# Optimization experiments

Measured on AMD Instinct MI355X. Metric: run time of the kernel, lower is better.

Reference implementation:

```python
import jax, jax.numpy as jnp
import numpy as np

SEQ_LEN = 8192
SIGMA = 2.0
COUNT_WEIGHT = 0.1
PEAK_PROB = 0.002  # ~16 peaks per sequence
LOG_CLAMP = -100.0  # torch F.binary_cross_entropy clamps log to -100


def setup_inputs() -> dict:
    key = jax.random.key(0)
    k1, k2 = jax.random.split(key)
    B = 32
    pred = jax.random.uniform(k1, (B, SEQ_LEN, 1), dtype=jnp.float32,
                              minval=1e-6, maxval=1.0 - 1e-6)
    # sparse binary peak indicator, as in radar pulse labels
    target = (jax.random.uniform(k2, (B, SEQ_LEN, 1)) < PEAK_PROB).astype(jnp.float32)
    return {"pred": pred, "target": target}


def _gaussian_target(target):
    # target: [B, T, 1]; original loops over every (b, t) peak and adds a
    # full-length gaussian centered at t. Vectorized: mask[B,T] @ K[T,T].
    T = target.shape[1]
    t_idx = jnp.arange(T, dtype=jnp.float32)
    K = jnp.exp(-0.5 * ((t_idx[None, :] - t_idx[:, None]) / SIGMA) ** 2)  # [T, T]
    mask = (target[:, :, 0] > 0).astype(jnp.float32)                      # [B, T]
    g = jnp.einsum("bt,ts->bs", mask, K)                                  # [B, T]
    return jnp.clip(g, 0.0, 1.0)[:, :, None]                              # [B, T, 1]


def reference(pred, target):
    gt = _gaussian_target(target)
    # binary_cross_entropy (mean reduction) with torch-style log clamping
    log_p = jnp.maximum(jnp.log(pred), LOG_CLAMP)
    log_1mp = jnp.maximum(jnp.log1p(-pred), LOG_CLAMP)
    bce_loss = -jnp.mean(gt * log_p + (1.0 - gt) * log_1mp)

    pred_peaks = (pred > 0.5).astype(jnp.float32)
    count_diff = jnp.abs(pred_peaks.sum(axis=1) - target.sum(axis=1))  # [B, 1]
    count_loss = COUNT_WEIGHT * jnp.mean(count_diff)

    total_loss = bce_loss + count_loss
    return total_loss, bce_loss, count_loss
```

## Files before the change

### kernel.cpp

```cpp
#include <hip/hip_runtime.h>


#define BATCH    32
#define SEQ_T    8192
#define CHUNK    1024
#define NWORK    (BATCH * (SEQ_T / CHUNK))
#define HALO     32
#define KTAB     67
#define MAXPEAKS 64
#define NTHREADS 256
#define FLAG_MAGIC 0x5CA1AB1E


__global__ __launch_bounds__(NTHREADS) void pulse_loss_one(
    const float* __restrict__ pred,
    const float* __restrict__ tgt,
    float* __restrict__ out,
    float* __restrict__ ws)
{
    const int tid = threadIdx.x;
    float* ws_f = ws;
    int*   ws_i = (int*)ws;

    if (blockIdx.x == 0) {
        int* flags = ws_i + 2 * NWORK;
        const int t = tid;

        while (__hip_atomic_load(&flags[t], __ATOMIC_ACQUIRE,
                                 __HIP_MEMORY_SCOPE_AGENT) != FLAG_MAGIC) {
            __builtin_amdgcn_s_sleep(2);
        }
        float bce = __hip_atomic_load(&ws_f[t], __ATOMIC_RELAXED,
                                      __HIP_MEMORY_SCOPE_AGENT);
        int   dc  = __hip_atomic_load(&ws_i[NWORK + t], __ATOMIC_RELAXED,
                                      __HIP_MEMORY_SCOPE_AGENT);
        __hip_atomic_store(&flags[t], 0, __ATOMIC_RELAXED,
                           __HIP_MEMORY_SCOPE_AGENT);

        dc += __shfl_down(dc, 4, 8);
        dc += __shfl_down(dc, 2, 8);
        dc += __shfl_down(dc, 1, 8);
        float ad = ((t & 7) == 0) ? fabsf((float)dc) : 0.0f;

        #pragma unroll
        for (int off = 32; off > 0; off >>= 1) {
            bce += __shfl_down(bce, off);
            ad  += __shfl_down(ad,  off);
        }

        __shared__ float s_b[4], s_a[4];
        const int wid  = t >> 6;
        const int lane = t & 63;
        if (lane == 0) { s_b[wid] = bce; s_a[wid] = ad; }
        __syncthreads();

        if (t == 0) {
            float sb = 0.0f, sd = 0.0f;
            #pragma unroll
            for (int w = 0; w < 4; ++w) { sb += s_b[w]; sd += s_a[w]; }
            float bce_loss   = -sb / (float)(BATCH * SEQ_T);
            float count_loss = 0.1f * sd / (float)BATCH;
            out[0] = bce_loss + count_loss;
            out[1] = bce_loss;
            out[2] = count_loss;
        }
        return;
    }

    const int blk = blockIdx.x - 1;
    const int b   = blk >> 3;
    const int c0  = (blk & 7) * CHUNK;
    const float* __restrict__ prow = pred + (size_t)b * SEQ_T;
    const float* __restrict__ trow = tgt  + (size_t)b * SEQ_T;

    __shared__ int   s_npeaks;
    __shared__ int   s_peaks[MAXPEAKS];
    __shared__ float s_K[KTAB];
    __shared__ float s_bce[NTHREADS / 64];
    __shared__ int   s_cnt[NTHREADS / 64];

    if (tid == 0) s_npeaks = 0;
    if (tid < KTAB) {
        float d = (float)(tid - 33);
        s_K[tid] = __expf(-0.125f * d * d);
    }
    __syncthreads();

    int cnt_t = 0;
    for (int i = tid; i < CHUNK + 2 * HALO; i += NTHREADS) {
        int gi = c0 - HALO + i;
        if (gi >= 0 && gi < SEQ_T) {
            if (trow[gi] > 0.0f) {
                int idx = atomicAdd(&s_npeaks, 1);
                if (idx < MAXPEAKS) s_peaks[idx] = gi;
                if (gi >= c0 && gi < c0 + CHUNK) cnt_t++;
            }
        }
    }
    __syncthreads();
    const int np = min(s_npeaks, MAXPEAKS);

    const float4 p4 = ((const float4*)(prow + c0))[tid];
    float bce  = 0.0f;
    int   dcnt = -cnt_t;
    #pragma unroll
    for (int j = 0; j < 4; ++j) {
        const float p = (j == 0) ? p4.x : (j == 1) ? p4.y : (j == 2) ? p4.z : p4.w;
        const int   i = c0 + tid * 4 + j;
        float g = 0.0f;
        for (int k = 0; k < np; ++k) {
            int d = i - s_peaks[k];
            d = min(max(d, -33), 33);
            g += s_K[d + 33];
        }
        g = fminf(g, 1.0f);
        float lp  = fmaxf(__logf(p),        -100.0f);
        float l1p = fmaxf(__logf(1.0f - p), -100.0f);
        bce  += l1p + g * (lp - l1p);
        dcnt += (p > 0.5f) ? 1 : 0;
    }

    #pragma unroll
    for (int off = 32; off > 0; off >>= 1) {
        bce  += __shfl_down(bce,  off);
        dcnt += __shfl_down(dcnt, off);
    }
    const int wid  = tid >> 6;
    const int lane = tid & 63;
    if (lane == 0) { s_bce[wid] = bce; s_cnt[wid] = dcnt; }
    __syncthreads();

    if (tid == 0) {
        float tb = 0.0f;
        int   tc = 0;
        #pragma unroll
        for (int w = 0; w < NTHREADS / 64; ++w) { tb += s_bce[w]; tc += s_cnt[w]; }
        __hip_atomic_store(&ws_f[blk], tb, __ATOMIC_RELAXED,
                           __HIP_MEMORY_SCOPE_AGENT);
        __hip_atomic_store(&ws_i[NWORK + blk], tc, __ATOMIC_RELAXED,
                           __HIP_MEMORY_SCOPE_AGENT);
        __hip_atomic_store(&ws_i[2 * NWORK + blk], FLAG_MAGIC, __ATOMIC_RELEASE,
                           __HIP_MEMORY_SCOPE_AGENT);
    }
}

extern "C" void kernel_launch(void* const* d_in, const int* in_sizes, int n_in,
                              void* d_out, int out_size, void* d_ws, size_t ws_size,
                              hipStream_t stream) {
    const float* pred = (const float*)d_in[0];
    const float* tgt  = (const float*)d_in[1];
    float*       out  = (float*)d_out;
    float*       ws   = (float*)d_ws;

    pulse_loss_one<<<dim3(NWORK + 1), dim3(NTHREADS), 0, stream>>>(
        pred, tgt, out, ws);
}
```

Measured before the change: 11.86 us.

## Vectorize target scan, merge gaussian loops, and fold log terms per thread

The strided scalar scan of targets is replaced by one float4 load per thread plus float4 halo loads from 16 threads, all issued before the first barrier so they overlap the kernel table setup. The per-element peak loop becomes one loop that accumulates four gaussian sums at once, sharing each shared-memory peak read. The four log(1-p) terms are folded into a single log of a product, and log(p) is evaluated only where the gaussian is nonzero, which drops the -100 clamp. The spin-wait sleep in the reducer block is also shortened. The exchange is a risk of underflow in the product of the 1-p values, and peak-index overflow now wraps instead of being dropped.

```diff
diff --git a/kernel.cpp b/kernel.cpp
--- a/kernel.cpp
+++ b/kernel.cpp
@@ -18,7 +18,7 @@
     float* __restrict__ out,
     float* __restrict__ ws)
 {
-    const int tid = threadIdx.x;
+    const int tid  = threadIdx.x;
     float* ws_f = ws;
     int*   ws_i = (int*)ws;
 
@@ -28,7 +28,7 @@
 
         while (__hip_atomic_load(&flags[t], __ATOMIC_ACQUIRE,
                                  __HIP_MEMORY_SCOPE_AGENT) != FLAG_MAGIC) {
-            __builtin_amdgcn_s_sleep(2);
+            __builtin_amdgcn_s_sleep(1);
         }
         float bce = __hip_atomic_load(&ws_f[t], __ATOMIC_RELAXED,
                                       __HIP_MEMORY_SCOPE_AGENT);
@@ -79,6 +79,17 @@
     __shared__ float s_bce[NTHREADS / 64];
     __shared__ int   s_cnt[NTHREADS / 64];
 
+    const int    ibase = c0 + tid * 4;
+    const float4 p4 = ((const float4*)(prow + c0))[tid];
+    const float4 t4 = ((const float4*)(trow + c0))[tid];
+    float4 h4 = make_float4(0.0f, 0.0f, 0.0f, 0.0f);
+    int    hbase = -1;
+    if (tid < 16) {
+        int h = (tid < 8) ? (c0 - HALO + tid * 4)
+                          : (c0 + CHUNK + (tid - 8) * 4);
+        if (h >= 0 && h < SEQ_T) { h4 = *(const float4*)(trow + h); hbase = h; }
+    }
+
     if (tid == 0) s_npeaks = 0;
     if (tid < KTAB) {
         float d = (float)(tid - 33);
@@ -87,38 +98,40 @@
     __syncthreads();
 
     int cnt_t = 0;
-    for (int i = tid; i < CHUNK + 2 * HALO; i += NTHREADS) {
-        int gi = c0 - HALO + i;
-        if (gi >= 0 && gi < SEQ_T) {
-            if (trow[gi] > 0.0f) {
-                int idx = atomicAdd(&s_npeaks, 1);
-                if (idx < MAXPEAKS) s_peaks[idx] = gi;
-                if (gi >= c0 && gi < c0 + CHUNK) cnt_t++;
-            }
-        }
+    if (t4.x > 0.0f) { s_peaks[atomicAdd(&s_npeaks, 1) & (MAXPEAKS - 1)] = ibase;     cnt_t++; }
+    if (t4.y > 0.0f) { s_peaks[atomicAdd(&s_npeaks, 1) & (MAXPEAKS - 1)] = ibase + 1; cnt_t++; }
+    if (t4.z > 0.0f) { s_peaks[atomicAdd(&s_npeaks, 1) & (MAXPEAKS - 1)] = ibase + 2; cnt_t++; }
+    if (t4.w > 0.0f) { s_peaks[atomicAdd(&s_npeaks, 1) & (MAXPEAKS - 1)] = ibase + 3; cnt_t++; }
+    if (hbase >= 0) {
+        if (h4.x > 0.0f) s_peaks[atomicAdd(&s_npeaks, 1) & (MAXPEAKS - 1)] = hbase;
+        if (h4.y > 0.0f) s_peaks[atomicAdd(&s_npeaks, 1) & (MAXPEAKS - 1)] = hbase + 1;
+        if (h4.z > 0.0f) s_peaks[atomicAdd(&s_npeaks, 1) & (MAXPEAKS - 1)] = hbase + 2;
+        if (h4.w > 0.0f) s_peaks[atomicAdd(&s_npeaks, 1) & (MAXPEAKS - 1)] = hbase + 3;
     }
     __syncthreads();
     const int np = min(s_npeaks, MAXPEAKS);
 
-    const float4 p4 = ((const float4*)(prow + c0))[tid];
-    float bce  = 0.0f;
-    int   dcnt = -cnt_t;
-    #pragma unroll
-    for (int j = 0; j < 4; ++j) {
-        const float p = (j == 0) ? p4.x : (j == 1) ? p4.y : (j == 2) ? p4.z : p4.w;
-        const int   i = c0 + tid * 4 + j;
-        float g = 0.0f;
-        for (int k = 0; k < np; ++k) {
-            int d = i - s_peaks[k];
-            d = min(max(d, -33), 33);
-            g += s_K[d + 33];
-        }
-        g = fminf(g, 1.0f);
-        float lp  = fmaxf(__logf(p),        -100.0f);
-        float l1p = fmaxf(__logf(1.0f - p), -100.0f);
-        bce  += l1p + g * (lp - l1p);
-        dcnt += (p > 0.5f) ? 1 : 0;
+    float g0 = 0.0f, g1 = 0.0f, g2 = 0.0f, g3 = 0.0f;
+    for (int k = 0; k < np; ++k) {
+        const int pk = ibase - s_peaks[k];
+        int d0 = min(max(pk,     -33), 33);
+        int d1 = min(max(pk + 1, -33), 33);
+        int d2 = min(max(pk + 2, -33), 33);
+        int d3 = min(max(pk + 3, -33), 33);
+        g0 += s_K[d0 + 33]; g1 += s_K[d1 + 33];
+        g2 += s_K[d2 + 33]; g3 += s_K[d3 + 33];
     }
+
+    const float q0 = 1.0f - p4.x, q1 = 1.0f - p4.y;
+    const float q2 = 1.0f - p4.z, q3 = 1.0f - p4.w;
+    float bce = __logf((q0 * q1) * (q2 * q3));
+    if (g0 > 0.0f) bce += fminf(g0, 1.0f) * (__logf(p4.x) - __logf(q0));
+    if (g1 > 0.0f) bce += fminf(g1, 1.0f) * (__logf(p4.y) - __logf(q1));
+    if (g2 > 0.0f) bce += fminf(g2, 1.0f) * (__logf(p4.z) - __logf(q2));
+    if (g3 > 0.0f) bce += fminf(g3, 1.0f) * (__logf(p4.w) - __logf(q3));
+
+    int dcnt = ((p4.x > 0.5f) ? 1 : 0) + ((p4.y > 0.5f) ? 1 : 0)
+             + ((p4.z > 0.5f) ? 1 : 0) + ((p4.w > 0.5f) ? 1 : 0) - cnt_t;
 
     #pragma unroll
     for (int off = 32; off > 0; off >>= 1) {
```

After: 11.63 us. -2.0%, faster.
